# Performance work log

Hardware: AMD Instinct MI355X
Metric: run time of the kernel (lower is better)

The kernel has to match this reference:

```python
import jax, jax.numpy as jnp
import numpy as np

B, HI, WI, DIM = 16, 64, 64, 256
HEADS, HEAD_DIM, NUM_MEM = 8, 32, 4
HID = HEADS * HEAD_DIM


def setup_inputs() -> dict:
    key = jax.random.key(0)
    ks = jax.random.split(key, 6)
    return {
        "x": jax.random.normal(ks[0], (B, HI, WI, DIM), jnp.float32),
        "gamma_in": jax.random.normal(ks[1], (DIM,), jnp.float32) * 0.02,
        "w_qkv": jax.random.normal(ks[2], (DIM, 3 * HID), jnp.float32) / np.sqrt(DIM),
        "b_qkv": jnp.zeros((3 * HID,), jnp.float32),
        "mem_kv": jax.random.normal(ks[3], (2, HEADS, NUM_MEM, HEAD_DIM), jnp.float32),
        "w_out": jax.random.normal(ks[4], (HID, DIM), jnp.float32) / np.sqrt(HID),
        "b_out": jnp.zeros((DIM,), jnp.float32),
        "gamma_out": jax.random.normal(ks[5], (DIM,), jnp.float32) * 0.02,
    }


def reference(x, gamma_in, w_qkv, b_qkv, mem_kv, w_out, b_out, gamma_out):
    b, h, w, c = x.shape
    n = h * w
    rms_scale = c ** 0.5
    attn_scale = HEAD_DIM ** -0.5

    # RMSNorm (as written in source: pure learned scaling)
    xn = x * (gamma_in + 1.0) * rms_scale

    # 1x1 conv == per-pixel linear projection
    qkv = xn @ w_qkv + b_qkv                       # (b, h, w, 3*HID)
    q, k, v = jnp.split(qkv, 3, axis=-1)

    def to_heads(t):                                # (b,h,w,HID) -> (b, heads, d, n)
        return t.reshape(b, n, HEADS, HEAD_DIM).transpose(0, 2, 3, 1)

    q, k, v = map(to_heads, (q, k, v))

    # memory kv: (heads, m, d) -> (b, heads, d, m), concat along sequence axis
    mk = jnp.broadcast_to(mem_kv[0].transpose(0, 2, 1)[None], (b, HEADS, HEAD_DIM, NUM_MEM))
    mv = jnp.broadcast_to(mem_kv[1].transpose(0, 2, 1)[None], (b, HEADS, HEAD_DIM, NUM_MEM))
    k = jnp.concatenate([mk, k], axis=-1)           # (b, heads, d, n+m)
    v = jnp.concatenate([mv, v], axis=-1)

    # feature-map attention: softmax q over feature dim, k over sequence dim
    q = jax.nn.softmax(q * attn_scale, axis=-2)     # source scales q before softmax
    k = jax.nn.softmax(k, axis=-1)

    context = jnp.einsum('bhdn,bhen->bhde', k, v)   # (b, heads, d, e) small
    out = jnp.einsum('bhde,bhdn->bhen', context, q) # (b, heads, e, n)

    out = out.transpose(0, 3, 1, 2).reshape(b, h, w, HID)
    y = out @ w_out + b_out                         # 1x1 output conv
    return y * (gamma_out + 1.0) * rms_scale        # output RMSNorm
```

## Files before the change

### kernel.cpp

```cpp
#include <hip/hip_runtime.h>
#include <hip/hip_bf16.h>

typedef __bf16 bf16_t;
typedef _Float16 fp16_t;
typedef _Float16 f16x8 __attribute__((ext_vector_type(8)));
typedef __bf16 bf16x8 __attribute__((ext_vector_type(8)));
typedef __bf16 bf16x4 __attribute__((ext_vector_type(4)));
typedef float f32x4 __attribute__((ext_vector_type(4)));

#define ATTN_SCALE 0.17677669529663687f
#define K_SHIFT 64.0f
#define Q_SHIFT 8.0f

__device__ __forceinline__ void gload16(const void* g, void* l) {
  __builtin_amdgcn_global_load_lds((const __attribute__((address_space(1))) void*)g,
                                   (__attribute__((address_space(3))) void*)l, 16, 0, 0);
}

__global__ __launch_bounds__(256) void prep_pack(
    const float* __restrict__ w_qkv, fp16_t* __restrict__ Bpack) {
  int idx = blockIdx.x * 256 + threadIdx.x;
  int l = idx & 63;
  int rest = idx >> 6;
  int f = rest & 3;
  int kk = (rest >> 2) & 7;
  int nt = rest >> 5;
  int n = nt * 64 + f * 16 + (l & 15);
  int k0 = kk * 32 + (l >> 4) * 8;
  f16x8 v;
#pragma unroll
  for (int e = 0; e < 8; ++e) v[e] = (fp16_t)w_qkv[(k0 + e) * 768 + n];
  ((f16x8*)Bpack)[idx] = v;
}

__global__ __launch_bounds__(256) void gemm_qvk_ctx(
    const float* __restrict__ x, const float* __restrict__ gamma_in,
    const fp16_t* __restrict__ Bpack, const float* __restrict__ bias,
    fp16_t* __restrict__ qe_out, float* __restrict__ part) {
  __shared__ fp16_t A[64 * 256];
  __shared__ bf16_t Pl[32 * 64];
  __shared__ bf16_t Vl[32 * 64];
  int t = threadIdx.x, l = t & 63, w = t >> 6;
  int lr = l >> 4, lc = l & 15;
  int bx = blockIdx.x;
  int m0 = bx * 64;

#pragma unroll
  for (int i = 0; i < 8; ++i) {
    int idx = i * 256 + t;
    int r = idx >> 5, c8 = idx & 31;
    const float* src = x + (size_t)(m0 + r) * 256 + c8 * 8;
    const float* gsc = gamma_in + c8 * 8;
    f16x8 hv;
#pragma unroll
    for (int j = 0; j < 8; ++j) hv[j] = (fp16_t)(src[j] * (gsc[j] + 1.f) * 16.f);
    *(f16x8*)&A[r * 256 + ((c8 ^ (r & 31)) * 8)] = hv;
  }
  __syncthreads();

  {
    const fp16_t* Bp = Bpack + (size_t)w * 16384;
    f32x4 acc[4][4];
#pragma unroll
    for (int mf = 0; mf < 4; ++mf)
#pragma unroll
      for (int nf = 0; nf < 4; ++nf) acc[mf][nf] = (f32x4){0.f, 0.f, 0.f, 0.f};
#pragma unroll
    for (int kk = 0; kk < 8; ++kk) {
      f16x8 af[4], bfr[4];
#pragma unroll
      for (int f = 0; f < 4; ++f) {
        int ra = f * 16 + lc;
        af[f] = *(const f16x8*)&A[ra * 256 + (((kk * 4 + lr) ^ (ra & 31)) * 8)];
        bfr[f] = *(const f16x8*)(Bp + (size_t)(kk * 4 + f) * 512 + l * 8);
      }
#pragma unroll
      for (int mf = 0; mf < 4; ++mf)
#pragma unroll
        for (int nf = 0; nf < 4; ++nf)
          acc[mf][nf] = __builtin_amdgcn_mfma_f32_16x16x32_f16(af[mf], bfr[nf], acc[mf][nf], 0, 0, 0);
    }
    int n0 = w * 64;
    float bq[4];
#pragma unroll
    for (int nf = 0; nf < 4; ++nf) bq[nf] = bias[n0 + nf * 16 + lc];
#pragma unroll
    for (int mf = 0; mf < 4; ++mf)
#pragma unroll
      for (int r = 0; r < 4; ++r) {
        int row = m0 + mf * 16 + lr * 4 + r;
#pragma unroll
        for (int nf = 0; nf < 4; ++nf) {
          float ql = (acc[mf][nf][r] + bq[nf]) * ATTN_SCALE;
          qe_out[(size_t)row * 256 + n0 + nf * 16 + lc] = (fp16_t)__expf(ql - Q_SHIFT);
        }
      }
  }

  bool isK = (w < 2);
  int rh = w & 1;
  int mf2 = w >> 1;
  int nf2 = w & 1;
  for (int ph = 0; ph < 8; ++ph) {
    int nt = (isK ? 4 : 8) + (ph >> 1);
    int chh = ph & 1;
    const fp16_t* Bp = Bpack + (size_t)nt * 16384;
    f32x4 acc[2][2];
#pragma unroll
    for (int mf = 0; mf < 2; ++mf)
#pragma unroll
      for (int nf = 0; nf < 2; ++nf) acc[mf][nf] = (f32x4){0.f, 0.f, 0.f, 0.f};
#pragma unroll
    for (int kk = 0; kk < 8; ++kk) {
      f16x8 af[2], bfr[2];
#pragma unroll
      for (int f = 0; f < 2; ++f) {
        int ra = rh * 32 + f * 16 + lc;
        af[f] = *(const f16x8*)&A[ra * 256 + (((kk * 4 + lr) ^ (ra & 31)) * 8)];
        bfr[f] = *(const f16x8*)(Bp + (size_t)(kk * 4 + chh * 2 + f) * 512 + l * 8);
      }
#pragma unroll
      for (int mf = 0; mf < 2; ++mf)
#pragma unroll
        for (int nf = 0; nf < 2; ++nf)
          acc[mf][nf] = __builtin_amdgcn_mfma_f32_16x16x32_f16(af[mf], bfr[nf], acc[mf][nf], 0, 0, 0);
    }
    int n0 = nt * 64 + chh * 32;
    float bv[2];
#pragma unroll
    for (int nf = 0; nf < 2; ++nf) bv[nf] = bias[n0 + nf * 16 + lc];
#pragma unroll
    for (int mf = 0; mf < 2; ++mf) {
#pragma unroll
      for (int nf = 0; nf < 2; ++nf) {
        int col = nf * 16 + lc;
        int row0 = rh * 32 + mf * 16 + lr * 4;
        bf16x4 pk;
#pragma unroll
        for (int r = 0; r < 4; ++r) {
          float val = acc[mf][nf][r] + bv[nf];
          pk[r] = isK ? (bf16_t)__expf(val - K_SHIFT) : (bf16_t)val;
        }
        int addr = col * 64 + ((((row0 >> 3) ^ (col & 7)) << 3) | (row0 & 7));
        if (isK) *(bf16x4*)&Pl[addr] = pk;
        else     *(bf16x4*)&Vl[addr] = pk;
      }
    }
    __syncthreads();

    {
      f32x4 sacc = (f32x4){0.f, 0.f, 0.f, 0.f};
      f32x4 zacc = (f32x4){0.f, 0.f, 0.f, 0.f};
      bf16x8 ones;
#pragma unroll
      for (int i = 0; i < 8; ++i) ones[i] = (bf16_t)1.0f;
#pragma unroll
      for (int kk = 0; kk < 2; ++kk) {
        int colA = mf2 * 16 + lc;
        bf16x8 ap = *(const bf16x8*)&Pl[colA * 64 + (((kk * 4 + lr) ^ (colA & 7)) << 3)];
        int colB = nf2 * 16 + lc;
        bf16x8 bvv = *(const bf16x8*)&Vl[colB * 64 + (((kk * 4 + lr) ^ (colB & 7)) << 3)];
        sacc = __builtin_amdgcn_mfma_f32_16x16x32_bf16(ap, bvv, sacc, 0, 0, 0);
        if (nf2 == 0)
          zacc = __builtin_amdgcn_mfma_f32_16x16x32_bf16(ap, ones, zacc, 0, 0, 0);
      }
      float* pp = part + (size_t)bx * 8448 + ph * 1056;
#pragma unroll
      for (int r = 0; r < 4; ++r) {
        int dd = mf2 * 16 + lr * 4 + r;
        pp[dd * 32 + nf2 * 16 + lc] = sacc[r];
        if (nf2 == 0 && lc == 0) pp[1024 + dd] = zacc[r];
      }
    }
    __syncthreads();
  }
}

__global__ __launch_bounds__(256) void build_wt(
    const float* __restrict__ part, const float* __restrict__ w_out,
    const float* __restrict__ mem_kv, fp16_t* __restrict__ Bpacky) {
  int bh = blockIdx.x;
  int b = bh >> 3, h = bh & 7;
  int t = threadIdx.x;
  __shared__ float S[32][32];
  __shared__ float Zr[32];
  __shared__ float W[32][256];
  for (int idx = t; idx < 1024; idx += 256) {
    float s = 0.f;
    for (int c = 0; c < 64; ++c) s += part[((size_t)(b * 64 + c)) * 8448 + h * 1056 + idx];
    S[idx >> 5][idx & 31] = s;
  }
  if (t < 32) {
    float zz = 0.f;
    for (int c = 0; c < 64; ++c) zz += part[((size_t)(b * 64 + c)) * 8448 + h * 1056 + 1024 + t];
    Zr[t] = zz;
  }
  for (int i = t; i < 32 * 256; i += 256) W[i >> 8][i & 255] = w_out[(h * 32 + (i >> 8)) * 256 + (i & 255)];
  __syncthreads();
  if (t < 32) {
    int dd = t;
    for (int m = 0; m < 4; ++m) {
      float p = __expf(mem_kv[h * 128 + m * 32 + dd] - K_SHIFT);
      Zr[dd] += p;
      for (int e = 0; e < 32; ++e) S[dd][e] += p * mem_kv[1024 + h * 128 + m * 32 + e];
    }
  }
  __syncthreads();
  int c = t;
  int nt = c >> 6, f = (c >> 4) & 3, lc = c & 15;
  for (int dd = 0; dd < 32; ++dd) {
    float acc = 0;
#pragma unroll 8
    for (int e = 0; e < 32; ++e) acc += S[dd][e] * W[e][c];
    int kcol = h * 32 + dd;
    int kk = kcol >> 5, lr = (kcol & 31) >> 3, e8 = kcol & 7;
    size_t addr = ((((size_t)(b * 4 + nt) * 8 + kk) * 4 + f) * 64 + (lr * 16 + lc)) * 8 + e8;
    Bpacky[addr] = (fp16_t)(acc / Zr[dd]);
  }
}

__global__ __launch_bounds__(256) void gemm_y(
    const fp16_t* __restrict__ qe, const fp16_t* __restrict__ Bpacky,
    const float* __restrict__ b_out, const float* __restrict__ gamma_out,
    float* __restrict__ y_out) {
  __shared__ fp16_t A[64 * 256];
  __shared__ float zbuf[64][8];
  int t = threadIdx.x, l = t & 63, w = t >> 6;
  int lr = l >> 4, lc = l & 15;
  int m0 = blockIdx.x * 64;
#pragma unroll
  for (int i = 0; i < 8; ++i) {
    int idx = i * 256 + t;
    int r = idx >> 5, cs = idx & 31;
    gload16(qe + (size_t)(m0 + r) * 256 + ((cs ^ (r & 31)) * 8), &A[idx * 8]);
  }
  __syncthreads();

#pragma unroll
  for (int pi = 0; pi < 2; ++pi) {
    int p = pi * 256 + t;
    int r = p >> 3, hh = p & 7;
    float zs = 0.f;
#pragma unroll
    for (int c = 0; c < 4; ++c) {
      int cs = (hh * 4 + c) ^ (r & 31);
      f16x8 vv = *(const f16x8*)&A[r * 256 + cs * 8];
#pragma unroll
      for (int j = 0; j < 8; ++j) zs += (float)vv[j];
    }
    zbuf[r][hh] = 1.f / zs;
  }
  __syncthreads();

#pragma unroll
  for (int i = 0; i < 8; ++i) {
    int idx = i * 256 + t;
    int r = idx >> 5, cs = idx & 31;
    int hh = (cs ^ (r & 31)) >> 2;
    float sc = zbuf[r][hh];
    f16x8 vv = *(const f16x8*)&A[idx * 8];
#pragma unroll
    for (int j = 0; j < 8; ++j) vv[j] = (fp16_t)((float)vv[j] * sc);
    *(f16x8*)&A[idx * 8] = vv;
  }
  __syncthreads();

  int n0 = w * 64;
  const fp16_t* Bp = Bpacky + (size_t)(m0 >> 12) * 65536 + (size_t)w * 16384;
  f32x4 acc[4][4];
#pragma unroll
  for (int mf = 0; mf < 4; ++mf)
#pragma unroll
    for (int nf = 0; nf < 4; ++nf) acc[mf][nf] = (f32x4){0.f, 0.f, 0.f, 0.f};
#pragma unroll
  for (int kk = 0; kk < 8; ++kk) {
    f16x8 af[4], bfr[4];
#pragma unroll
    for (int f = 0; f < 4; ++f) {
      int ra = f * 16 + lc;
      af[f] = *(const f16x8*)&A[ra * 256 + (((kk * 4 + lr) ^ (ra & 31)) * 8)];
      bfr[f] = *(const f16x8*)(Bp + (size_t)(kk * 4 + f) * 512 + l * 8);
    }
#pragma unroll
    for (int mf = 0; mf < 4; ++mf)
#pragma unroll
      for (int nf = 0; nf < 4; ++nf)
        acc[mf][nf] = __builtin_amdgcn_mfma_f32_16x16x32_f16(af[mf], bfr[nf], acc[mf][nf], 0, 0, 0);
  }
  float bv[4], gv[4];
#pragma unroll
  for (int nf = 0; nf < 4; ++nf) {
    int c = n0 + nf * 16 + lc;
    bv[nf] = b_out[c];
    gv[nf] = (gamma_out[c] + 1.f) * 16.f;
  }
#pragma unroll
  for (int mf = 0; mf < 4; ++mf)
#pragma unroll
    for (int r = 0; r < 4; ++r) {
      int row = m0 + mf * 16 + lr * 4 + r;
#pragma unroll
      for (int nf = 0; nf < 4; ++nf)
        y_out[(size_t)row * 256 + n0 + nf * 16 + lc] = (acc[mf][nf][r] + bv[nf]) * gv[nf];
    }
}

extern "C" void kernel_launch(void* const* d_in, const int* in_sizes, int n_in,
                              void* d_out, int out_size, void* d_ws, size_t ws_size,
                              hipStream_t stream) {
  const float* x        = (const float*)d_in[0];
  const float* gamma_in = (const float*)d_in[1];
  const float* w_qkv    = (const float*)d_in[2];
  const float* b_qkv    = (const float*)d_in[3];
  const float* mem_kv   = (const float*)d_in[4];
  const float* w_out    = (const float*)d_in[5];
  const float* b_out    = (const float*)d_in[6];
  const float* gamma_out= (const float*)d_in[7];
  float* y = (float*)d_out;

  char* ws = (char*)d_ws;
  fp16_t* qe     = (fp16_t*)(ws);
  fp16_t* Bpack  = (fp16_t*)(ws + 33554432);
  fp16_t* Bpacky = (fp16_t*)(ws + 33947648);
  float*  part   = (float*)(ws + 36044800);

  prep_pack<<<96, 256, 0, stream>>>(w_qkv, Bpack);
  gemm_qvk_ctx<<<1024, 256, 0, stream>>>(x, gamma_in, Bpack, b_qkv, qe, part);
  build_wt<<<128, 256, 0, stream>>>(part, w_out, mem_kv, Bpacky);
  gemm_y<<<1024, 256, 0, stream>>>(qe, Bpacky, b_out, gamma_out, y);
}
```

Baseline: 135.8 us.

## Prefetch packed QKV weights into per-wave LDS ring with async global-to-LDS loads

Each wave now streams its slice of the packed weight matrix into a private 4-slot LDS ring using global_load_lds, issued several k-steps ahead, with explicit vmcnt waits before each MFMA step. This replaces direct global reads of the B fragments inside the inner loop and aims to hide global memory latency behind the MFMA work. It also raises wave priority around the MFMA blocks in all GEMM loops. The extra 32 KB of LDS per block may reduce occupancy, and the hand-written vmcnt counting must line up with the other outstanding loads.

```diff
diff --git a/kernel.cpp b/kernel.cpp
--- a/kernel.cpp
+++ b/kernel.cpp
@@ -38,12 +38,23 @@
     const fp16_t* __restrict__ Bpack, const float* __restrict__ bias,
     fp16_t* __restrict__ qe_out, float* __restrict__ part) {
   __shared__ fp16_t A[64 * 256];
+  __shared__ fp16_t Bl[4][4][1024];
   __shared__ bf16_t Pl[32 * 64];
   __shared__ bf16_t Vl[32 * 64];
   int t = threadIdx.x, l = t & 63, w = t >> 6;
   int lr = l >> 4, lc = l & 15;
   int bx = blockIdx.x;
   int m0 = bx * 64;
+  fp16_t* myBl = &Bl[w][0][0];
+
+  auto issue2 = [&](const fp16_t* src, int slot) {
+    gload16(src + l * 8, myBl + slot * 1024 + l * 8);
+    gload16(src + 512 + l * 8, myBl + slot * 1024 + 512 + l * 8);
+  };
+
+  const fp16_t* Bq = Bpack + (size_t)w * 16384;
+#pragma unroll
+  for (int g = 0; g < 4; ++g) issue2(Bq + g * 1024, g);
 
 #pragma unroll
   for (int i = 0; i < 8; ++i) {
@@ -59,7 +70,6 @@
   __syncthreads();
 
   {
-    const fp16_t* Bp = Bpack + (size_t)w * 16384;
     f32x4 acc[4][4];
 #pragma unroll
     for (int mf = 0; mf < 4; ++mf)
@@ -67,18 +77,27 @@
       for (int nf = 0; nf < 4; ++nf) acc[mf][nf] = (f32x4){0.f, 0.f, 0.f, 0.f};
 #pragma unroll
     for (int kk = 0; kk < 8; ++kk) {
+      if (kk <= 6) asm volatile("s_waitcnt vmcnt(4)" ::: "memory");
+      else         asm volatile("s_waitcnt vmcnt(0)" ::: "memory");
+      __builtin_amdgcn_sched_barrier(0);
       f16x8 af[4], bfr[4];
 #pragma unroll
       for (int f = 0; f < 4; ++f) {
         int ra = f * 16 + lc;
         af[f] = *(const f16x8*)&A[ra * 256 + (((kk * 4 + lr) ^ (ra & 31)) * 8)];
-        bfr[f] = *(const f16x8*)(Bp + (size_t)(kk * 4 + f) * 512 + l * 8);
-      }
+        bfr[f] = *(const f16x8*)(myBl + (((2 * kk + (f >> 1)) & 3) * 1024) + (f & 1) * 512 + l * 8);
+      }
+      __builtin_amdgcn_s_setprio(1);
 #pragma unroll
       for (int mf = 0; mf < 4; ++mf)
 #pragma unroll
         for (int nf = 0; nf < 4; ++nf)
           acc[mf][nf] = __builtin_amdgcn_mfma_f32_16x16x32_f16(af[mf], bfr[nf], acc[mf][nf], 0, 0, 0);
+      __builtin_amdgcn_s_setprio(0);
+      if (kk <= 5) {
+        issue2(Bq + (2 * kk + 4) * 1024, (2 * kk + 4) & 3);
+        issue2(Bq + (2 * kk + 5) * 1024, (2 * kk + 5) & 3);
+      }
     }
     int n0 = w * 64;
     float bq[4];
@@ -104,7 +123,9 @@
   for (int ph = 0; ph < 8; ++ph) {
     int nt = (isK ? 4 : 8) + (ph >> 1);
     int chh = ph & 1;
-    const fp16_t* Bp = Bpack + (size_t)nt * 16384;
+    const fp16_t* Bp = Bpack + (size_t)nt * 16384 + chh * 1024;
+#pragma unroll
+    for (int g = 0; g < 3; ++g) issue2(Bp + g * 2048, g);
     f32x4 acc[2][2];
 #pragma unroll
     for (int mf = 0; mf < 2; ++mf)
@@ -112,18 +133,25 @@
       for (int nf = 0; nf < 2; ++nf) acc[mf][nf] = (f32x4){0.f, 0.f, 0.f, 0.f};
 #pragma unroll
     for (int kk = 0; kk < 8; ++kk) {
+      if (kk <= 5)      asm volatile("s_waitcnt vmcnt(4)" ::: "memory");
+      else if (kk == 6) asm volatile("s_waitcnt vmcnt(2)" ::: "memory");
+      else              asm volatile("s_waitcnt vmcnt(0)" ::: "memory");
+      __builtin_amdgcn_sched_barrier(0);
       f16x8 af[2], bfr[2];
 #pragma unroll
       for (int f = 0; f < 2; ++f) {
         int ra = rh * 32 + f * 16 + lc;
         af[f] = *(const f16x8*)&A[ra * 256 + (((kk * 4 + lr) ^ (ra & 31)) * 8)];
-        bfr[f] = *(const f16x8*)(Bp + (size_t)(kk * 4 + chh * 2 + f) * 512 + l * 8);
-      }
+        bfr[f] = *(const f16x8*)(myBl + ((kk & 3) * 1024) + f * 512 + l * 8);
+      }
+      __builtin_amdgcn_s_setprio(1);
 #pragma unroll
       for (int mf = 0; mf < 2; ++mf)
 #pragma unroll
         for (int nf = 0; nf < 2; ++nf)
           acc[mf][nf] = __builtin_amdgcn_mfma_f32_16x16x32_f16(af[mf], bfr[nf], acc[mf][nf], 0, 0, 0);
+      __builtin_amdgcn_s_setprio(0);
+      if (kk + 3 <= 7) issue2(Bp + (kk + 3) * 2048, (kk + 3) & 3);
     }
     int n0 = nt * 64 + chh * 32;
     float bv[2];
@@ -160,9 +188,11 @@
         bf16x8 ap = *(const bf16x8*)&Pl[colA * 64 + (((kk * 4 + lr) ^ (colA & 7)) << 3)];
         int colB = nf2 * 16 + lc;
         bf16x8 bvv = *(const bf16x8*)&Vl[colB * 64 + (((kk * 4 + lr) ^ (colB & 7)) << 3)];
+        __builtin_amdgcn_s_setprio(1);
         sacc = __builtin_amdgcn_mfma_f32_16x16x32_bf16(ap, bvv, sacc, 0, 0, 0);
         if (nf2 == 0)
           zacc = __builtin_amdgcn_mfma_f32_16x16x32_bf16(ap, ones, zacc, 0, 0, 0);
+        __builtin_amdgcn_s_setprio(0);
       }
       float* pp = part + (size_t)bx * 8448 + ph * 1056;
 #pragma unroll
@@ -281,11 +311,13 @@
       af[f] = *(const f16x8*)&A[ra * 256 + (((kk * 4 + lr) ^ (ra & 31)) * 8)];
       bfr[f] = *(const f16x8*)(Bp + (size_t)(kk * 4 + f) * 512 + l * 8);
     }
+    __builtin_amdgcn_s_setprio(1);
 #pragma unroll
     for (int mf = 0; mf < 4; ++mf)
 #pragma unroll
       for (int nf = 0; nf < 4; ++nf)
         acc[mf][nf] = __builtin_amdgcn_mfma_f32_16x16x32_f16(af[mf], bfr[nf], acc[mf][nf], 0, 0, 0);
+    __builtin_amdgcn_s_setprio(0);
   }
   float bv[4], gv[4];
 #pragma unroll
```

Result: no change. 134.7 us (-0.8%).
